# Kernel tuning notes

Hardware: AMD Instinct MI355X
Metric: run time of the kernel (lower is better)

The kernel has to match this reference:

```python
import jax, jax.numpy as jnp
import numpy as np

B, N, M, C, K = 2, 8192, 4096, 64, 16
HID = 256
EPS_BN = 1e-5


def setup_inputs() -> dict:
    key = jax.random.key(0)
    ks = jax.random.split(key, 16)
    def rn(i, shape, scale=1.0):
        return jax.random.normal(ks[i], shape, jnp.float32) * scale
    return {
        "pcl": rn(0, (B, M, 3)),
        "pcl_noise": rn(1, (B, N, 3)),
        "feature": rn(2, (B, M, C)),
        # MLP_CONV (2d 1x1): 6 -> 256 (BN+ReLU) -> C
        "w2a": rn(3, (HID, 6), 0.3), "b2a": rn(4, (HID,), 0.1),
        "g2a": 1.0 + rn(5, (HID,), 0.1), "bt2a": rn(6, (HID,), 0.1),
        "w2b": rn(7, (C, HID), 0.1), "b2b": rn(8, (C,), 0.1),
        # MLP_CONV_1d: 3C -> C (BN+ReLU) -> C
        "w1a": rn(9, (C, 3 * C), 0.1), "b1a": rn(10, (C,), 0.1),
        "g1a": 1.0 + rn(11, (C,), 0.1), "bt1a": rn(12, (C,), 0.1),
        "w1b": rn(13, (C, C), 0.1), "b1b": rn(14, (C,), 0.1),
    }


def _sqdist(x, y):  # [B,n,3],[B,m,3] -> [B,n,m]
    return (jnp.sum(x * x, -1, keepdims=True)
            - 2.0 * jnp.einsum('bnc,bmc->bnm', x, y)
            + jnp.sum(y * y, -1)[:, None, :])


def _gather(x, idx):  # x [B,M,D], idx [B,...] -> [B,...,D]
    return jax.vmap(lambda xb, ib: xb[ib])(x, idx)


def _bn(h, g, b):  # inference BatchNorm: running mean 0, var 1
    return h * (g / jnp.sqrt(1.0 + EPS_BN)) + b


def reference(pcl, pcl_noise, feature, w2a, b2a, g2a, bt2a, w2b, b2b,
              w1a, b1a, g1a, bt1a, w1b, b1b):
    # nearest clean point for each noisy point (knn_points K=1)
    close_idx = jnp.argmin(_sqdist(pcl_noise, pcl), axis=-1)          # [B,N]
    close_point = _gather(pcl, close_idx)                             # [B,N,3]
    # K nearest neighbors of close_point within pcl (dil_knn, d=1)
    _, idx = jax.lax.top_k(-_sqdist(close_point, pcl), K)             # [B,N,K]
    knn_points = _gather(pcl, idx)[:, :, 1:, :]                       # [B,N,K-1,3]
    knn_feat = _gather(feature, idx)[:, :, 1:, :]                     # [B,N,K-1,C]
    close_feat = _gather(feature, close_idx)                          # [B,N,C]

    delta = knn_points - pcl_noise[:, :, None, :]                     # [B,N,K-1,3]
    dst = jnp.linalg.norm(delta, axis=-1)                             # [B,N,K-1]
    e = jnp.exp(-10.0 * dst)
    weight = e / (jnp.sum(e, -1, keepdims=True) + 1e-7)               # [B,N,K-1]

    cp = jnp.broadcast_to(close_point[:, :, None, :], delta.shape)
    delta_points = jnp.concatenate([delta, cp], axis=-1)              # [B,N,K-1,6]

    # MLP_CONV2 (1x1 convs over channel dim)
    h = jnp.einsum('bnkc,oc->bnko', delta_points, w2a) + b2a
    h = jax.nn.relu(_bn(h, g2a, bt2a))
    pf = jnp.einsum('bnkc,oc->bnko', h, w2b) + b2b                    # [B,N,K-1,C]

    point_feature = jnp.einsum('bnk,bnkc->bnc', weight, pf)           # [B,N,C]
    co_feature = jnp.einsum('bnk,bnkc->bnc', weight, knn_feat)        # [B,N,C]
    df = jnp.concatenate([close_feat, co_feature, point_feature], -1)  # [B,N,3C]

    # MLP_CONV_1d
    h1 = jnp.einsum('bnc,oc->bno', df, w1a) + b1a
    h1 = jax.nn.relu(_bn(h1, g1a, bt1a))
    return jnp.einsum('bnc,oc->bno', h1, w1b) + b1b                   # [B,N,C]
```

## Files before the change

### kernel.cpp

```cpp
#include <hip/hip_runtime.h>
#include <float.h>

typedef unsigned short u16;
typedef unsigned int u32;
typedef unsigned char u8;

typedef float f32x4 __attribute__((ext_vector_type(4)));
typedef short bh8   __attribute__((ext_vector_type(8)));

__device__ __forceinline__ float bf(u16 u) { return __uint_as_float(((u32)u) << 16); }
__device__ __forceinline__ u16 f2bf(float v) {
    u32 x = __float_as_uint(v);
    u32 r = x + 0x7fffu + ((x >> 16) & 1u);
    return (u16)(r >> 16);
}
__device__ __forceinline__ int detect_f32(const void* probe) {
    const u16* u = (const u16*)probe;
    u16 v = u[(threadIdx.x & 63) * 2];
    int e = (int)((v >> 7) & 0xFF);
    int moderate = (e >= 100) && (e <= 140);
    return __popcll(__ballot(moderate)) < 48;
}
__device__ __forceinline__ float ldv(int f32, const void* p, int i) {
    return f32 ? ((const float*)p)[i] : bf(((const u16*)p)[i]);
}
__device__ __forceinline__ float dot3(float x0, float x1, float x2,
                                      float y0, float y1, float y2) {
    return __fmaf_rn(x2, y2, __fmaf_rn(x1, y1, __fmul_rn(x0, y0)));
}
__device__ __forceinline__ float qdist(float x0, float x1, float x2, float sx, float4 p) {
    float dot = dot3(x0, x1, x2, p.x, p.y, p.z);
    return __fadd_rn(__fsub_rn(sx, __fmul_rn(2.0f, dot)), p.w);
}
__device__ __forceinline__ u32 mkey32(float d) {
    u32 f = __float_as_uint(d);
    return f ^ (u32)((((int)f) >> 31) | 0x80000000);
}
__device__ __forceinline__ bh8 ldb(const void* p) { return *(const bh8*)p; }
__device__ __forceinline__ f32x4 mfma16(bh8 a, bh8 b, f32x4 c) {
    return __builtin_amdgcn_mfma_f32_16x16x32_bf16(a, b, c, 0, 0, 0);
}

__device__ __forceinline__ void knn_fallback(const float4* __restrict__ src,
                                             float x0, float x1, float x2, float sx,
                                             int q, u16* __restrict__ knn, int lane) {
    u32 k0=~0u,k1=~0u,k2=~0u,k3=~0u,k4=~0u,k5=~0u,k6=~0u,k7=~0u,
        k8=~0u,k9=~0u,k10=~0u,k11=~0u,k12=~0u,k13=~0u,k14=~0u,k15=~0u;
    u32 i0r=0,i1r=0,i2r=0,i3r=0,i4r=0,i5r=0,i6r=0,i7r=0,
        i8r=0,i9r=0,i10r=0,i11r=0,i12r=0,i13r=0,i14r=0,i15r=0;
    for (int j = 0; j < 64; ++j) {
        int cin = (j << 6) + lane;
        float d = qdist(x0, x1, x2, sx, src[cin]);
        u32 v = mkey32(d); u32 vi = (u32)cin;
        if (v < k15) {
            { u32 c_=(v<k0); u32 nk=c_?v:k0; u32 nv=c_?k0:v; u32 ni=c_?vi:i0r; u32 nj=c_?i0r:vi; k0=nk;i0r=ni;v=nv;vi=nj; }
            { u32 c_=(v<k1); u32 nk=c_?v:k1; u32 nv=c_?k1:v; u32 ni=c_?vi:i1r; u32 nj=c_?i1r:vi; k1=nk;i1r=ni;v=nv;vi=nj; }
            { u32 c_=(v<k2); u32 nk=c_?v:k2; u32 nv=c_?k2:v; u32 ni=c_?vi:i2r; u32 nj=c_?i2r:vi; k2=nk;i2r=ni;v=nv;vi=nj; }
            { u32 c_=(v<k3); u32 nk=c_?v:k3; u32 nv=c_?k3:v; u32 ni=c_?vi:i3r; u32 nj=c_?i3r:vi; k3=nk;i3r=ni;v=nv;vi=nj; }
            { u32 c_=(v<k4); u32 nk=c_?v:k4; u32 nv=c_?k4:v; u32 ni=c_?vi:i4r; u32 nj=c_?i4r:vi; k4=nk;i4r=ni;v=nv;vi=nj; }
            { u32 c_=(v<k5); u32 nk=c_?v:k5; u32 nv=c_?k5:v; u32 ni=c_?vi:i5r; u32 nj=c_?i5r:vi; k5=nk;i5r=ni;v=nv;vi=nj; }
            { u32 c_=(v<k6); u32 nk=c_?v:k6; u32 nv=c_?k6:v; u32 ni=c_?vi:i6r; u32 nj=c_?i6r:vi; k6=nk;i6r=ni;v=nv;vi=nj; }
            { u32 c_=(v<k7); u32 nk=c_?v:k7; u32 nv=c_?k7:v; u32 ni=c_?vi:i7r; u32 nj=c_?i7r:vi; k7=nk;i7r=ni;v=nv;vi=nj; }
            { u32 c_=(v<k8); u32 nk=c_?v:k8; u32 nv=c_?k8:v; u32 ni=c_?vi:i8r; u32 nj=c_?i8r:vi; k8=nk;i8r=ni;v=nv;vi=nj; }
            { u32 c_=(v<k9); u32 nk=c_?v:k9; u32 nv=c_?k9:v; u32 ni=c_?vi:i9r; u32 nj=c_?i9r:vi; k9=nk;i9r=ni;v=nv;vi=nj; }
            { u32 c_=(v<k10); u32 nk=c_?v:k10; u32 nv=c_?k10:v; u32 ni=c_?vi:i10r; u32 nj=c_?i10r:vi; k10=nk;i10r=ni;v=nv;vi=nj; }
            { u32 c_=(v<k11); u32 nk=c_?v:k11; u32 nv=c_?k11:v; u32 ni=c_?vi:i11r; u32 nj=c_?i11r:vi; k11=nk;i11r=ni;v=nv;vi=nj; }
            { u32 c_=(v<k12); u32 nk=c_?v:k12; u32 nv=c_?k12:v; u32 ni=c_?vi:i12r; u32 nj=c_?i12r:vi; k12=nk;i12r=ni;v=nv;vi=nj; }
            { u32 c_=(v<k13); u32 nk=c_?v:k13; u32 nv=c_?k13:v; u32 ni=c_?vi:i13r; u32 nj=c_?i13r:vi; k13=nk;i13r=ni;v=nv;vi=nj; }
            { u32 c_=(v<k14); u32 nk=c_?v:k14; u32 nv=c_?k14:v; u32 ni=c_?vi:i14r; u32 nj=c_?i14r:vi; k14=nk;i14r=ni;v=nv;vi=nj; }
            { u32 c_=(v<k15); u32 nk=c_?v:k15; u32 nv=c_?k15:v; u32 ni=c_?vi:i15r; u32 nj=c_?i15r:vi; k15=nk;i15r=ni;v=nv;vi=nj; }
        }
    }
    u32 myres = 0;
    for (int o = 0; o < 16; ++o) {
        u32 bk = k0, bi2 = i0r;
#pragma unroll
        for (int m = 32; m >= 1; m >>= 1) {
            u32 ok = __shfl_xor(bk, m), oi = __shfl_xor(bi2, m);
            if (ok < bk || (ok == bk && oi < bi2)) { bk = ok; bi2 = oi; }
        }
        if (lane == o) myres = bi2;
        if (k0 == bk && i0r == bi2) {
            k0=k1; i0r=i1r; k1=k2; i1r=i2r; k2=k3; i2r=i3r; k3=k4; i3r=i4r;
            k4=k5; i4r=i5r; k5=k6; i5r=i6r; k6=k7; i6r=i7r; k7=k8; i7r=i8r;
            k8=k9; i8r=i9r; k9=k10; i9r=i10r; k10=k11; i10r=i11r; k11=k12; i11r=i12r;
            k12=k13; i12r=i13r; k13=k14; i13r=i14r; k14=k15; i14r=i15r;
            k15=~0u; i15r=0xFFFFu;
        }
    }
    if (lane < 16) knn[((size_t)q << 4) + lane] = (u16)myres;
}

__global__ __launch_bounds__(256) void k_pre(const void* __restrict__ probe,
                                             const void* __restrict__ w2b,
                                             const void* __restrict__ w1a,
                                             const void* __restrict__ w1b,
                                             u32* __restrict__ canonb,
                                             const void* __restrict__ pcl,
                                             float4* __restrict__ pcl4) {
    int f32 = detect_f32(probe);
    int bx = blockIdx.x, t = threadIdx.x;
    if (bx < 64) {
        int ix = bx * 256 + t;
        const void* src; int j;
        if (ix < 8192)       { src = w2b; j = ix; }
        else if (ix < 14336) { src = w1a; j = ix - 8192; }
        else                 { src = w1b; j = ix - 14336; }
        u32 out;
        if (f32) {
            const float* f = (const float*)src;
            out = ((u32)f2bf(f[2*j+1]) << 16) | (u32)f2bf(f[2*j]);
        } else {
            const u16* su = (const u16*)src;
            out = ((u32)su[2*j+1] << 16) | (u32)su[2*j];
        }
        canonb[ix] = out;
    } else {
        int i = (bx - 64) * 256 + t;
        float x = ldv(f32, pcl, i*3+0), y = ldv(f32, pcl, i*3+1), z = ldv(f32, pcl, i*3+2);
        float s = __fadd_rn(__fadd_rn(__fmul_rn(x,x), __fmul_rn(y,y)), __fmul_rn(z,z));
        pcl4[i] = make_float4(x, y, z, s);
    }
}

__global__ __launch_bounds__(256) void k_sel(const float4* __restrict__ pcl4,
                                             const void* __restrict__ noise,
                                             u16* __restrict__ cidx,
                                             u16* __restrict__ knn) {
    __shared__ __align__(16) char arena[32768];
    int bx = blockIdx.x;
    int r5 = bx % 5, c5 = bx / 5;
    int t = threadIdx.x, lane = t & 63, wv = t >> 6;

    if (r5 == 0) {
        float4* tile = (float4*)arena;
        int f32 = detect_f32(noise);
        int g = t >> 4, s = t & 15;
        int q = c5 * 16 + g;
        int b = q >> 13;
        const float4* src = pcl4 + ((size_t)b << 12);
        float x0 = ldv(f32, noise, q*3+0), x1 = ldv(f32, noise, q*3+1), x2 = ldv(f32, noise, q*3+2);
        float sx = __fadd_rn(__fadd_rn(__fmul_rn(x0,x0), __fmul_rn(x1,x1)), __fmul_rn(x2,x2));
        float bd = FLT_MAX; int bi = 0;
        for (int ch = 0; ch < 2; ++ch) {
            __syncthreads();
#pragma unroll
            for (int i = 0; i < 8; ++i) { int ix = t + (i << 8); tile[ix] = src[(ch << 11) + ix]; }
            __syncthreads();
            for (int j = 0; j < 128; ++j) {
                int cl = (j << 4) + s;
                float4 p = tile[cl];
                float d = qdist(x0, x1, x2, sx, p);
                int c = (ch << 11) + cl;
                if (d < bd) { bd = d; bi = c; }
            }
        }
#pragma unroll
        for (int m = 8; m >= 1; m >>= 1) {
            float od = __shfl_xor(bd, m);
            int   oi = __shfl_xor(bi, m);
            if (od < bd || (od == bd && oi < bi)) { bd = od; bi = oi; }
        }
        if (s == 0) cidx[q] = (u16)(bi & 4095);
        return;
    }

    u8*  bins0 = (u8*)arena;
    u8*  bins1 = (u8*)(arena + 4096);
    u32* hist0 = (u32*)(arena + 8192);
    u32* hist1 = (u32*)(arena + 9216);
    u32* skey0 = (u32*)(arena + 10240);
    u32* skey1 = (u32*)(arena + 11264);
    u16* sidx0 = (u16*)(arena + 12288);
    u16* sidx1 = (u16*)(arena + 12800);
    float* rmn0 = (float*)(arena + 13312);
    float* rmx0 = (float*)(arena + 13328);
    float* rmn1 = (float*)(arena + 13344);
    float* rmx1 = (float*)(arena + 13360);
    u32* scnt0 = (u32*)(arena + 13376);
    u32* scnt1 = (u32*)(arena + 13380);
    int* ibst0 = (int*)(arena + 13384);
    int* ibst1 = (int*)(arena + 13388);

    int qp = c5 * 4 + (r5 - 1);
    int q0 = qp << 1, q1 = q0 | 1;
    int b = q0 >> 12;
    const float4* src = pcl4 + ((size_t)b << 12);
    float4 Q0 = src[q0 & 4095];
    float4 Q1 = src[q1 & 4095];
    float ax0 = Q0.x, ax1 = Q0.y, ax2 = Q0.z, asx = Q0.w;
    float bx0 = Q1.x, bx1 = Q1.y, bx2 = Q1.z, bsx = Q1.w;
    hist0[t] = 0; hist1[t] = 0;
    if (t == 0) { *scnt0 = 0; *scnt1 = 0; }
    {
        float4 p = src[t << 4];
        float da = qdist(ax0, ax1, ax2, asx, p);
        float db = qdist(bx0, bx1, bx2, bsx, p);
        float mn0 = da, mx0 = da, mn1 = db, mx1 = db;
#pragma unroll
        for (int m = 32; m >= 1; m >>= 1) {
            mn0 = fminf(mn0, __shfl_xor(mn0, m));
            mx0 = fmaxf(mx0, __shfl_xor(mx0, m));
            mn1 = fminf(mn1, __shfl_xor(mn1, m));
            mx1 = fmaxf(mx1, __shfl_xor(mx1, m));
        }
        if (lane == 0) { rmn0[wv] = mn0; rmx0[wv] = mx0; rmn1[wv] = mn1; rmx1[wv] = mx1; }
    }
    __syncthreads();
    float dmn0 = fminf(fminf(rmn0[0], rmn0[1]), fminf(rmn0[2], rmn0[3]));
    float dmx0 = fmaxf(fmaxf(rmx0[0], rmx0[1]), fmaxf(rmx0[2], rmx0[3]));
    float sc0f = 1024.0f / fmaxf(dmx0 - dmn0, 1e-20f);
    float dmn1 = fminf(fminf(rmn1[0], rmn1[1]), fminf(rmn1[2], rmn1[3]));
    float dmx1 = fmaxf(fmaxf(rmx1[0], rmx1[1]), fmaxf(rmx1[2], rmx1[3]));
    float sc1f = 1024.0f / fmaxf(dmx1 - dmn1, 1e-20f);
#pragma unroll 4
    for (int j = 0; j < 16; ++j) {
        int cin = (j << 8) + t;
        float4 p = src[cin];
        float d0 = qdist(ax0, ax1, ax2, asx, p);
        float d1 = qdist(bx0, bx1, bx2, bsx, p);
        int bn0 = (int)fminf(fmaxf((d0 - dmn0) * sc0f, 0.0f), 255.0f);
        int bn1 = (int)fminf(fmaxf((d1 - dmn1) * sc1f, 0.0f), 255.0f);
        bins0[cin] = (u8)bn0;
        bins1[cin] = (u8)bn1;
        if (bn0 < 255) atomicAdd(&hist0[bn0], 1u);
        if (bn1 < 255) atomicAdd(&hist1[bn1], 1u);
    }
    __syncthreads();
    if (wv < 2) {
        u32* hh = wv ? hist1 : hist0;
        u32 c0 = hh[4*lane], c1 = hh[4*lane+1];
        u32 c2 = hh[4*lane+2], c3 = hh[4*lane+3];
        u32 loc = c0 + c1 + c2 + c3;
        u32 x = loc;
#pragma unroll
        for (int off = 1; off < 64; off <<= 1) { u32 v = __shfl_up(x, off); if (lane >= off) x += v; }
        u32 excl = x - loc;
        int cand = 999;
        if (excl + c0 >= 16u) cand = 4*lane;
        else if (excl + c0 + c1 >= 16u) cand = 4*lane + 1;
        else if (excl + c0 + c1 + c2 >= 16u) cand = 4*lane + 2;
        else if (excl + loc >= 16u) cand = 4*lane + 3;
#pragma unroll
        for (int m = 32; m >= 1; m >>= 1) cand = min(cand, __shfl_xor(cand, m));
        if (lane == 0) { if (wv) *ibst1 = cand; else *ibst0 = cand; }
    }
    __syncthreads();
    int bstar0 = *ibst0, bstar1 = *ibst1;
#pragma unroll
    for (int j = 0; j < 16; ++j) {
        int cin = (j << 8) + t;
        int s0 = (int)bins0[cin] <= bstar0;
        int s1 = (int)bins1[cin] <= bstar1;
        if (s0 | s1) {
            float4 p = src[cin];
            if (s0) {
                u32 pos = atomicAdd(scnt0, 1u);
                if (pos < 256u) {
                    float d = qdist(ax0, ax1, ax2, asx, p);
                    skey0[pos] = mkey32(d); sidx0[pos] = (u16)cin;
                }
            }
            if (s1) {
                u32 pos = atomicAdd(scnt1, 1u);
                if (pos < 256u) {
                    float d = qdist(bx0, bx1, bx2, bsx, p);
                    skey1[pos] = mkey32(d); sidx1[pos] = (u16)cin;
                }
            }
        }
    }
    __syncthreads();
    u32 n0 = *scnt0, n1 = *scnt1;
    if (t < 128) {
        if (n0 <= 256u) {
            for (u32 e = (u32)t; e < n0; e += 128u) {
                u32 k = skey0[e]; u32 i = (u32)sidx0[e];
                int rank = 0;
                for (u32 j = 0; j < n0; ++j) {
                    u32 kj = skey0[j]; u32 ij = (u32)sidx0[j];
                    rank += (kj < k) || (kj == k && ij < i);
                }
                if (rank < 16) knn[((size_t)q0 << 4) + rank] = (u16)i;
            }
        } else if (wv == 0) {
            knn_fallback(src, ax0, ax1, ax2, asx, q0, knn, lane);
        }
    } else {
        if (n1 <= 256u) {
            for (u32 e = (u32)(t - 128); e < n1; e += 128u) {
                u32 k = skey1[e]; u32 i = (u32)sidx1[e];
                int rank = 0;
                for (u32 j = 0; j < n1; ++j) {
                    u32 kj = skey1[j]; u32 ij = (u32)sidx1[j];
                    rank += (kj < k) || (kj == k && ij < i);
                }
                if (rank < 16) knn[((size_t)q1 << 4) + rank] = (u16)i;
            }
        } else if (wv == 2) {
            knn_fallback(src, bx0, bx1, bx2, bsx, q1, knn, lane);
        }
    }
}

__global__ __launch_bounds__(256) void k_tail(const float4* __restrict__ pcl4,
                                              const void* __restrict__ noise,
                                              const void* __restrict__ feat,
                                              const u16* __restrict__ cidx,
                                              const u16* __restrict__ knn,
                                              const void* __restrict__ w2a,
                                              const void* __restrict__ b2a,
                                              const void* __restrict__ g2a,
                                              const void* __restrict__ bt2a,
                                              const u32* __restrict__ canonb,
                                              const void* __restrict__ b2b,
                                              const void* __restrict__ b1a,
                                              const void* __restrict__ g1a,
                                              const void* __restrict__ bt1a,
                                              const void* __restrict__ b1b,
                                              void* __restrict__ outp) {
    __shared__ __align__(16) char arena[39744];
    char* dpb_hi = arena;
    char* dpb_lo = arena + 4352;
    char* wbt    = arena + 8704;
    char* wsbp   = arena + 9984;
    u16*  jbuf   = (u16*)(arena + 10048);
    char* hbm_   = arena + 10560;
    char* dfm    = arena + 27200;
    char* h1m    = arena;

    int f32 = detect_f32(noise);
    int t = threadIdx.x, lane = t & 63, wv = t >> 6;
    int g = lane >> 4, l15 = lane & 15;
    int qbb = blockIdx.x * 16;
    int o_lane = wv * 16 + l15;
    const float rbn = 1.0f / sqrtf(1.0f + 1e-5f);
    const char* cb = (const char*)canonb;
    const f32x4 zero4 = {0.f, 0.f, 0.f, 0.f};

    float of2r[4];
    bh8 wH[4];
#pragma unroll
    for (int j = 0; j < 4; ++j) {
        int oh = wv*64 + j*16 + l15;
        float sc = ldv(f32, g2a, oh) * rbn;
        of2r[j] = ldv(f32, b2a, oh) * sc + ldv(f32, bt2a, oh);
        bh8 wz = (bh8){0,0,0,0,0,0,0,0};
        if (g < 3) {
#pragma unroll
            for (int c = 0; c < 6; ++c) {
                float wval = ldv(f32, w2a, oh*6 + c) * sc;
                u16 h = f2bf(wval);
                u16 e = (g == 2) ? f2bf(wval - bf(h)) : h;
                wz[c] = (short)e;
            }
        }
        wH[j] = wz;
    }
    float s1o  = ldv(f32, g1a, o_lane) * rbn;
    float o1o  = ldv(f32, b1a, o_lane) * s1o + ldv(f32, bt1a, o_lane);
    float b2bo = ldv(f32, b2b, o_lane);
    float b1fo = ldv(f32, b1b, o_lane);

    {
        int s = lane & 15;
        int ql = wv*4 + (lane >> 4);
        int q = qbb + ql;
        int pbase = (q >> 13) << 12;
        int ci = ((int)cidx[q]) & 4095;
        float4 cp = pcl4[pbase + ci];
        float x0 = ldv(f32, noise, q*3+0), x1 = ldv(f32, noise, q*3+1), x2 = ldv(f32, noise, q*3+2);
        float e = 0.0f;
        if (s >= 1) {
            int jk = ((int)knn[(size_t)(pbase + ci) * 16 + s]) & 4095;
            float4 p = pcl4[pbase + jk];
            float d0 = p.x - x0, d1 = p.y - x1, d2 = p.z - x2;
            float dst = sqrtf(__fadd_rn(__fadd_rn(__fmul_rn(d0,d0), __fmul_rn(d1,d1)), __fmul_rn(d2,d2)));
            e = expf(-10.0f * dst);
            float v6[6] = {d0, d1, d2, cp.x, cp.y, cp.z};
            bh8 HW = (bh8){0,0,0,0,0,0,0,0};
            bh8 LW = (bh8){0,0,0,0,0,0,0,0};
#pragma unroll
            for (int c = 0; c < 6; ++c) {
                u16 hh = f2bf(v6[c]);
                u16 ll = f2bf(v6[c] - bf(hh));
                HW[c] = (short)hh;
                LW[c] = (short)ll;
            }
            *(bh8*)(dpb_hi + (ql*17 + s)*16) = HW;
            *(bh8*)(dpb_lo + (ql*17 + s)*16) = LW;
            jbuf[ql*16 + s] = (u16)jk;
        }
        float es = e;
#pragma unroll
        for (int m = 8; m >= 1; m >>= 1) es += __shfl_xor(es, m, 16);
        float den = es + 1e-7f;
        if (s >= 1) *(float*)(wbt + s*80 + ql*4) = e / den;
        if (s == 0) *(float*)(wsbp + ql*4) = es / den;
    }
    __syncthreads();

#pragma unroll
    for (int qq = 0; qq < 4; ++qq) {
        int qloc = wv*4 + qq;
        int q = qbb + qloc;
        int pbase = (q >> 13) << 12;
        int ci = ((int)cidx[q]) & 4095;
        size_t fcb = ((size_t)(pbase + ci)) << 6;
        float c0, c1 = 0.0f;
        if (f32) {
            const float* ff = (const float*)feat;
            c0 = ff[fcb + lane];
#pragma unroll
            for (int k = 1; k < 16; ++k) {
                float wk = *(const float*)(wbt + k*80 + qloc*4);
                c1 += wk * ff[(((size_t)(pbase + (int)jbuf[qloc*16 + k])) << 6) + lane];
            }
        } else {
            const u16* fb = (const u16*)feat;
            c0 = bf(fb[fcb + lane]);
#pragma unroll
            for (int k = 1; k < 16; ++k) {
                float wk = *(const float*)(wbt + k*80 + qloc*4);
                c1 += wk * bf(fb[(((size_t)(pbase + (int)jbuf[qloc*16 + k])) << 6) + lane]);
            }
        }
        char* dr = dfm + qloc*784;
        u16 h0 = f2bf(c0); u16 l0 = f2bf(c0 - bf(h0));
        u16 h1v = f2bf(c1); u16 l1v = f2bf(c1 - bf(h1v));
        *(u16*)(dr + (size_t)lane*2)         = h0;
        *(u16*)(dr + (size_t)(192+lane)*2)   = l0;
        *(u16*)(dr + (size_t)(64+lane)*2)    = h1v;
        *(u16*)(dr + (size_t)(256+lane)*2)   = l1v;
    }

    {
        f32x4 hba[4];
#pragma unroll
        for (int j = 0; j < 4; ++j) hba[j] = zero4;
#pragma unroll 2
        for (int k = 1; k < 16; ++k) {
            bh8 af;
            if (g < 3) {
                const char* base = (g == 1) ? dpb_lo : dpb_hi;
                af = ldb(base + (l15*17 + k)*16);
            } else {
                af = (bh8){0,0,0,0,0,0,0,0};
            }
            f32x4 wk4 = *(const f32x4*)(wbt + k*80 + g*16);
#pragma unroll
            for (int j = 0; j < 4; ++j) {
                f32x4 d = mfma16(af, wH[j], zero4);
#pragma unroll
                for (int r = 0; r < 4; ++r)
                    hba[j][r] += wk4[r] * fmaxf(d[r] + of2r[j], 0.0f);
            }
        }
#pragma unroll
        for (int j = 0; j < 4; ++j)
#pragma unroll
            for (int r = 0; r < 4; ++r) {
                int q = g*4 + r;
                int o = wv*64 + j*16 + l15;
                float x = hba[j][r];
                u16 h = f2bf(x); u16 l = f2bf(x - bf(h));
                *(u16*)(hbm_ + q*1040 + (size_t)o*2)       = h;
                *(u16*)(hbm_ + q*1040 + 512 + (size_t)o*2) = l;
            }
    }
    __syncthreads();

    {
        f32x4 acA = zero4, acB = zero4;
#pragma unroll 2
        for (int ks = 0; ks < 8; ++ks) {
            bh8 bw = ldb(cb + (size_t)o_lane*512 + ks*64 + g*16);
            bh8 aH = ldb(hbm_ + l15*1040 + ks*64 + g*16);
            bh8 aL = ldb(hbm_ + l15*1040 + 512 + ks*64 + g*16);
            acA = mfma16(aH, bw, acA);
            acB = mfma16(aL, bw, acB);
        }
        f32x4 wsb4 = *(const f32x4*)(wsbp + g*16);
#pragma unroll
        for (int r = 0; r < 4; ++r) {
            int q = g*4 + r;
            float pf = acA[r] + acB[r] + b2bo * wsb4[r];
            u16 h = f2bf(pf); u16 l = f2bf(pf - bf(h));
            *(u16*)(dfm + q*784 + (size_t)(128 + o_lane)*2) = h;
            *(u16*)(dfm + q*784 + (size_t)(320 + o_lane)*2) = l;
        }
    }
    __syncthreads();

    {
        f32x4 acA = zero4, acB = zero4;
#pragma unroll 2
        for (int ks = 0; ks < 6; ++ks) {
            bh8 bw = ldb(cb + 32768 + (size_t)o_lane*384 + ks*64 + g*16);
            bh8 aH = ldb(dfm + l15*784 + ks*64 + g*16);
            bh8 aL = ldb(dfm + l15*784 + 384 + ks*64 + g*16);
            acA = mfma16(aH, bw, acA);
            acB = mfma16(aL, bw, acB);
        }
#pragma unroll
        for (int r = 0; r < 4; ++r) {
            int q = g*4 + r;
            float z = (acA[r] + acB[r]) * s1o + o1o;
            z = fmaxf(z, 0.0f);
            u16 h = f2bf(z); u16 l = f2bf(z - bf(h));
            *(u16*)(h1m + q*272 + (size_t)o_lane*2)       = h;
            *(u16*)(h1m + q*272 + 128 + (size_t)o_lane*2) = l;
        }
    }
    __syncthreads();

    {
        bh8 bw0 = ldb(cb + 57344 + (size_t)o_lane*128 + g*16);
        bh8 bw1 = ldb(cb + 57344 + (size_t)o_lane*128 + 64 + g*16);
        f32x4 ac = zero4;
        { bh8 a = ldb(h1m + l15*272 +   0 + g*16); ac = mfma16(a, bw0, ac); }
        { bh8 a = ldb(h1m + l15*272 +  64 + g*16); ac = mfma16(a, bw1, ac); }
        { bh8 a = ldb(h1m + l15*272 + 128 + g*16); ac = mfma16(a, bw0, ac); }
        { bh8 a = ldb(h1m + l15*272 + 192 + g*16); ac = mfma16(a, bw1, ac); }
#pragma unroll
        for (int r = 0; r < 4; ++r) {
            int q = g*4 + r;
            float ov = ac[r] + b1fo;
            size_t ob = ((size_t)(qbb + q) << 6) + o_lane;
            if (f32) ((float*)outp)[ob] = ov;
            else     ((u16*)outp)[ob]   = f2bf(ov);
        }
    }
}

extern "C" void kernel_launch(void* const* d_in, const int* in_sizes, int n_in,
                              void* d_out, int out_size, void* d_ws, size_t ws_size,
                              hipStream_t stream) {
    const void* pcl   = d_in[0];
    const void* noise = d_in[1];
    const void* feat  = d_in[2];
    const void* w2a   = d_in[3];
    const void* b2a   = d_in[4];
    const void* g2a   = d_in[5];
    const void* bt2a  = d_in[6];
    const void* w2b   = d_in[7];
    const void* b2b   = d_in[8];
    const void* w1a   = d_in[9];
    const void* b1a   = d_in[10];
    const void* g1a   = d_in[11];
    const void* bt1a  = d_in[12];
    const void* w1b   = d_in[13];
    const void* b1b   = d_in[14];

    char* ws = (char*)d_ws;
    float4* pcl4 = (float4*)ws;
    u16* cidx = (u16*)(ws + 131072);
    u16* knn  = (u16*)(ws + 163840);
    u32* canonb = (u32*)(ws + 425984);

    k_pre  <<<96,   256, 0, stream>>>(noise, w2b, w1a, w1b, canonb, pcl, pcl4);
    k_sel  <<<5120, 256, 0, stream>>>(pcl4, noise, cidx, knn);
    k_tail <<<1024, 256, 0, stream>>>(pcl4, noise, feat, cidx, knn,
                                      w2a, b2a, g2a, bt2a, canonb, b2b,
                                      b1a, g1a, bt1a, b1b, d_out);
}
```

Baseline: 205.6 us.

## Process four kNN query points per block in k_sel instead of two

Each kNN-selection block now handles four clean-point queries instead of two. Every candidate point loaded from global memory is reused for four distance computations, and the grid shrinks from 5120 to 3072 blocks. Shared memory per block grows to about 27KB for four bin/histogram/key arrays. Each wave now ranks one query's candidates on its own, so the rank loop uses 64 lanes per query instead of 128, and register pressure rises, which may lower occupancy.

```diff
diff --git a/kernel.cpp b/kernel.cpp
--- a/kernel.cpp
+++ b/kernel.cpp
@@ -129,14 +129,14 @@
                                              u16* __restrict__ knn) {
     __shared__ __align__(16) char arena[32768];
     int bx = blockIdx.x;
-    int r5 = bx % 5, c5 = bx / 5;
+    int r3 = bx % 3, c3 = bx / 3;
     int t = threadIdx.x, lane = t & 63, wv = t >> 6;
 
-    if (r5 == 0) {
+    if (r3 == 0) {
         float4* tile = (float4*)arena;
         int f32 = detect_f32(noise);
         int g = t >> 4, s = t & 15;
-        int q = c5 * 16 + g;
+        int q = c3 * 16 + g;
         int b = q >> 13;
         const float4* src = pcl4 + ((size_t)b << 12);
         float x0 = ldv(f32, noise, q*3+0), x1 = ldv(f32, noise, q*3+1), x2 = ldv(f32, noise, q*3+2);
@@ -165,70 +165,82 @@
         return;
     }
 
-    u8*  bins0 = (u8*)arena;
-    u8*  bins1 = (u8*)(arena + 4096);
-    u32* hist0 = (u32*)(arena + 8192);
-    u32* hist1 = (u32*)(arena + 9216);
-    u32* skey0 = (u32*)(arena + 10240);
-    u32* skey1 = (u32*)(arena + 11264);
-    u16* sidx0 = (u16*)(arena + 12288);
-    u16* sidx1 = (u16*)(arena + 12800);
-    float* rmn0 = (float*)(arena + 13312);
-    float* rmx0 = (float*)(arena + 13328);
-    float* rmn1 = (float*)(arena + 13344);
-    float* rmx1 = (float*)(arena + 13360);
-    u32* scnt0 = (u32*)(arena + 13376);
-    u32* scnt1 = (u32*)(arena + 13380);
-    int* ibst0 = (int*)(arena + 13384);
-    int* ibst1 = (int*)(arena + 13388);
-
-    int qp = c5 * 4 + (r5 - 1);
-    int q0 = qp << 1, q1 = q0 | 1;
+    u8*  binsA = (u8*)arena;
+    u32* histA = (u32*)(arena + 16384);
+    u32* skeyA = (u32*)(arena + 20480);
+    u16* sidxA = (u16*)(arena + 24576);
+    float* rmnA = (float*)(arena + 26624);
+    float* rmxA = (float*)(arena + 26688);
+    u32* scntA = (u32*)(arena + 26752);
+    int* ibstA = (int*)(arena + 26768);
+
+    int id = c3 * 2 + (r3 - 1);
+    int q0 = id << 2;
     int b = q0 >> 12;
     const float4* src = pcl4 + ((size_t)b << 12);
-    float4 Q0 = src[q0 & 4095];
-    float4 Q1 = src[q1 & 4095];
-    float ax0 = Q0.x, ax1 = Q0.y, ax2 = Q0.z, asx = Q0.w;
-    float bx0 = Q1.x, bx1 = Q1.y, bx2 = Q1.z, bsx = Q1.w;
-    hist0[t] = 0; hist1[t] = 0;
-    if (t == 0) { *scnt0 = 0; *scnt1 = 0; }
+    int qm = q0 & 4095;
+    float4 Q0 = src[qm], Q1 = src[qm+1], Q2 = src[qm+2], Q3 = src[qm+3];
+    float qx0=Q0.x, qy0=Q0.y, qz0=Q0.z, qs0=Q0.w;
+    float qx1=Q1.x, qy1=Q1.y, qz1=Q1.z, qs1=Q1.w;
+    float qx2=Q2.x, qy2=Q2.y, qz2=Q2.z, qs2=Q2.w;
+    float qx3=Q3.x, qy3=Q3.y, qz3=Q3.z, qs3=Q3.w;
+#pragma unroll
+    for (int qi = 0; qi < 4; ++qi) histA[(qi << 8) + t] = 0;
+    if (t < 4) scntA[t] = 0;
     {
         float4 p = src[t << 4];
-        float da = qdist(ax0, ax1, ax2, asx, p);
-        float db = qdist(bx0, bx1, bx2, bsx, p);
-        float mn0 = da, mx0 = da, mn1 = db, mx1 = db;
+        float d0 = qdist(qx0,qy0,qz0,qs0,p);
+        float d1 = qdist(qx1,qy1,qz1,qs1,p);
+        float d2 = qdist(qx2,qy2,qz2,qs2,p);
+        float d3 = qdist(qx3,qy3,qz3,qs3,p);
+        float mn0=d0,mx0=d0, mn1=d1,mx1=d1, mn2=d2,mx2=d2, mn3=d3,mx3=d3;
 #pragma unroll
         for (int m = 32; m >= 1; m >>= 1) {
-            mn0 = fminf(mn0, __shfl_xor(mn0, m));
-            mx0 = fmaxf(mx0, __shfl_xor(mx0, m));
-            mn1 = fminf(mn1, __shfl_xor(mn1, m));
-            mx1 = fmaxf(mx1, __shfl_xor(mx1, m));
-        }
-        if (lane == 0) { rmn0[wv] = mn0; rmx0[wv] = mx0; rmn1[wv] = mn1; rmx1[wv] = mx1; }
-    }
-    __syncthreads();
-    float dmn0 = fminf(fminf(rmn0[0], rmn0[1]), fminf(rmn0[2], rmn0[3]));
-    float dmx0 = fmaxf(fmaxf(rmx0[0], rmx0[1]), fmaxf(rmx0[2], rmx0[3]));
-    float sc0f = 1024.0f / fmaxf(dmx0 - dmn0, 1e-20f);
-    float dmn1 = fminf(fminf(rmn1[0], rmn1[1]), fminf(rmn1[2], rmn1[3]));
-    float dmx1 = fmaxf(fmaxf(rmx1[0], rmx1[1]), fmaxf(rmx1[2], rmx1[3]));
-    float sc1f = 1024.0f / fmaxf(dmx1 - dmn1, 1e-20f);
-#pragma unroll 4
+            mn0 = fminf(mn0, __shfl_xor(mn0, m)); mx0 = fmaxf(mx0, __shfl_xor(mx0, m));
+            mn1 = fminf(mn1, __shfl_xor(mn1, m)); mx1 = fmaxf(mx1, __shfl_xor(mx1, m));
+            mn2 = fminf(mn2, __shfl_xor(mn2, m)); mx2 = fmaxf(mx2, __shfl_xor(mx2, m));
+            mn3 = fminf(mn3, __shfl_xor(mn3, m)); mx3 = fmaxf(mx3, __shfl_xor(mx3, m));
+        }
+        if (lane == 0) {
+            rmnA[wv] = mn0;      rmxA[wv] = mx0;
+            rmnA[4+wv] = mn1;    rmxA[4+wv] = mx1;
+            rmnA[8+wv] = mn2;    rmxA[8+wv] = mx2;
+            rmnA[12+wv] = mn3;   rmxA[12+wv] = mx3;
+        }
+    }
+    __syncthreads();
+    float dmn0 = fminf(fminf(rmnA[0],rmnA[1]),fminf(rmnA[2],rmnA[3]));
+    float sc0  = 1024.0f / fmaxf(fmaxf(fmaxf(rmxA[0],rmxA[1]),fmaxf(rmxA[2],rmxA[3])) - dmn0, 1e-20f);
+    float dmn1 = fminf(fminf(rmnA[4],rmnA[5]),fminf(rmnA[6],rmnA[7]));
+    float sc1  = 1024.0f / fmaxf(fmaxf(fmaxf(rmxA[4],rmxA[5]),fmaxf(rmxA[6],rmxA[7])) - dmn1, 1e-20f);
+    float dmn2 = fminf(fminf(rmnA[8],rmnA[9]),fminf(rmnA[10],rmnA[11]));
+    float sc2  = 1024.0f / fmaxf(fmaxf(fmaxf(rmxA[8],rmxA[9]),fmaxf(rmxA[10],rmxA[11])) - dmn2, 1e-20f);
+    float dmn3 = fminf(fminf(rmnA[12],rmnA[13]),fminf(rmnA[14],rmnA[15]));
+    float sc3  = 1024.0f / fmaxf(fmaxf(fmaxf(rmxA[12],rmxA[13]),fmaxf(rmxA[14],rmxA[15])) - dmn3, 1e-20f);
+#pragma unroll 8
     for (int j = 0; j < 16; ++j) {
         int cin = (j << 8) + t;
         float4 p = src[cin];
-        float d0 = qdist(ax0, ax1, ax2, asx, p);
-        float d1 = qdist(bx0, bx1, bx2, bsx, p);
-        int bn0 = (int)fminf(fmaxf((d0 - dmn0) * sc0f, 0.0f), 255.0f);
-        int bn1 = (int)fminf(fmaxf((d1 - dmn1) * sc1f, 0.0f), 255.0f);
-        bins0[cin] = (u8)bn0;
-        bins1[cin] = (u8)bn1;
-        if (bn0 < 255) atomicAdd(&hist0[bn0], 1u);
-        if (bn1 < 255) atomicAdd(&hist1[bn1], 1u);
-    }
-    __syncthreads();
-    if (wv < 2) {
-        u32* hh = wv ? hist1 : hist0;
+        float d0 = qdist(qx0,qy0,qz0,qs0,p);
+        float d1 = qdist(qx1,qy1,qz1,qs1,p);
+        float d2 = qdist(qx2,qy2,qz2,qs2,p);
+        float d3 = qdist(qx3,qy3,qz3,qs3,p);
+        int bn0 = (int)fminf(fmaxf((d0 - dmn0) * sc0, 0.0f), 255.0f);
+        int bn1 = (int)fminf(fmaxf((d1 - dmn1) * sc1, 0.0f), 255.0f);
+        int bn2 = (int)fminf(fmaxf((d2 - dmn2) * sc2, 0.0f), 255.0f);
+        int bn3 = (int)fminf(fmaxf((d3 - dmn3) * sc3, 0.0f), 255.0f);
+        binsA[cin]         = (u8)bn0;
+        binsA[4096 + cin]  = (u8)bn1;
+        binsA[8192 + cin]  = (u8)bn2;
+        binsA[12288 + cin] = (u8)bn3;
+        if (bn0 < 255) atomicAdd(&histA[bn0], 1u);
+        if (bn1 < 255) atomicAdd(&histA[256 + bn1], 1u);
+        if (bn2 < 255) atomicAdd(&histA[512 + bn2], 1u);
+        if (bn3 < 255) atomicAdd(&histA[768 + bn3], 1u);
+    }
+    __syncthreads();
+    {
+        u32* hh = histA + (wv << 8);
         u32 c0 = hh[4*lane], c1 = hh[4*lane+1];
         u32 c2 = hh[4*lane+2], c3 = hh[4*lane+3];
         u32 loc = c0 + c1 + c2 + c3;
@@ -243,62 +255,60 @@
         else if (excl + loc >= 16u) cand = 4*lane + 3;
 #pragma unroll
         for (int m = 32; m >= 1; m >>= 1) cand = min(cand, __shfl_xor(cand, m));
-        if (lane == 0) { if (wv) *ibst1 = cand; else *ibst0 = cand; }
-    }
-    __syncthreads();
-    int bstar0 = *ibst0, bstar1 = *ibst1;
-#pragma unroll
+        if (lane == 0) ibstA[wv] = cand;
+    }
+    __syncthreads();
+    int bs0 = ibstA[0], bs1 = ibstA[1], bs2 = ibstA[2], bs3 = ibstA[3];
+#pragma unroll 4
     for (int j = 0; j < 16; ++j) {
         int cin = (j << 8) + t;
-        int s0 = (int)bins0[cin] <= bstar0;
-        int s1 = (int)bins1[cin] <= bstar1;
-        if (s0 | s1) {
+        int s0 = (int)binsA[cin]         <= bs0;
+        int s1 = (int)binsA[4096 + cin]  <= bs1;
+        int s2 = (int)binsA[8192 + cin]  <= bs2;
+        int s3 = (int)binsA[12288 + cin] <= bs3;
+        if (s0 | s1 | s2 | s3) {
             float4 p = src[cin];
             if (s0) {
-                u32 pos = atomicAdd(scnt0, 1u);
-                if (pos < 256u) {
-                    float d = qdist(ax0, ax1, ax2, asx, p);
-                    skey0[pos] = mkey32(d); sidx0[pos] = (u16)cin;
-                }
+                u32 pos = atomicAdd(&scntA[0], 1u);
+                if (pos < 256u) { skeyA[pos] = mkey32(qdist(qx0,qy0,qz0,qs0,p)); sidxA[pos] = (u16)cin; }
             }
             if (s1) {
-                u32 pos = atomicAdd(scnt1, 1u);
-                if (pos < 256u) {
-                    float d = qdist(bx0, bx1, bx2, bsx, p);
-                    skey1[pos] = mkey32(d); sidx1[pos] = (u16)cin;
-                }
-            }
-        }
-    }
-    __syncthreads();
-    u32 n0 = *scnt0, n1 = *scnt1;
-    if (t < 128) {
-        if (n0 <= 256u) {
-            for (u32 e = (u32)t; e < n0; e += 128u) {
-                u32 k = skey0[e]; u32 i = (u32)sidx0[e];
+                u32 pos = atomicAdd(&scntA[1], 1u);
+                if (pos < 256u) { skeyA[256+pos] = mkey32(qdist(qx1,qy1,qz1,qs1,p)); sidxA[256+pos] = (u16)cin; }
+            }
+            if (s2) {
+                u32 pos = atomicAdd(&scntA[2], 1u);
+                if (pos < 256u) { skeyA[512+pos] = mkey32(qdist(qx2,qy2,qz2,qs2,p)); sidxA[512+pos] = (u16)cin; }
+            }
+            if (s3) {
+                u32 pos = atomicAdd(&scntA[3], 1u);
+                if (pos < 256u) { skeyA[768+pos] = mkey32(qdist(qx3,qy3,qz3,qs3,p)); sidxA[768+pos] = (u16)cin; }
+            }
+        }
+    }
+    __syncthreads();
+    {
+        u32 nq = scntA[wv];
+        u32* sk = skeyA + (wv << 8);
+        u16* si = sidxA + (wv << 8);
+        int myq = q0 + wv;
+        if (nq <= 256u) {
+            for (u32 e = (u32)lane; e < nq; e += 64u) {
+                u32 k = sk[e]; u32 i = (u32)si[e];
                 int rank = 0;
-                for (u32 j = 0; j < n0; ++j) {
-                    u32 kj = skey0[j]; u32 ij = (u32)sidx0[j];
+                for (u32 jj = 0; jj < nq; ++jj) {
+                    u32 kj = sk[jj]; u32 ij = (u32)si[jj];
                     rank += (kj < k) || (kj == k && ij < i);
                 }
-                if (rank < 16) knn[((size_t)q0 << 4) + rank] = (u16)i;
-            }
-        } else if (wv == 0) {
-            knn_fallback(src, ax0, ax1, ax2, asx, q0, knn, lane);
-        }
-    } else {
-        if (n1 <= 256u) {
-            for (u32 e = (u32)(t - 128); e < n1; e += 128u) {
-                u32 k = skey1[e]; u32 i = (u32)sidx1[e];
-                int rank = 0;
-                for (u32 j = 0; j < n1; ++j) {
-                    u32 kj = skey1[j]; u32 ij = (u32)sidx1[j];
-                    rank += (kj < k) || (kj == k && ij < i);
-                }
-                if (rank < 16) knn[((size_t)q1 << 4) + rank] = (u16)i;
-            }
-        } else if (wv == 2) {
-            knn_fallback(src, bx0, bx1, bx2, bsx, q1, knn, lane);
+                if (rank < 16) knn[((size_t)myq << 4) + rank] = (u16)i;
+            }
+        } else {
+            float X, Y, Z, S;
+            if (wv == 0)      { X = qx0; Y = qy0; Z = qz0; S = qs0; }
+            else if (wv == 1) { X = qx1; Y = qy1; Z = qz1; S = qs1; }
+            else if (wv == 2) { X = qx2; Y = qy2; Z = qz2; S = qs2; }
+            else              { X = qx3; Y = qy3; Z = qz3; S = qs3; }
+            knn_fallback(src, X, Y, Z, S, myq, knn, lane);
         }
     }
 }
@@ -559,7 +569,7 @@
     u32* canonb = (u32*)(ws + 425984);
 
     k_pre  <<<96,   256, 0, stream>>>(noise, w2b, w1a, w1b, canonb, pcl, pcl4);
-    k_sel  <<<5120, 256, 0, stream>>>(pcl4, noise, cidx, knn);
+    k_sel  <<<3072, 256, 0, stream>>>(pcl4, noise, cidx, knn);
     k_tail <<<1024, 256, 0, stream>>>(pcl4, noise, feat, cidx, knn,
                                       w2a, b2a, g2a, bt2a, canonb, b2b,
                                       b1a, g1a, bt1a, b1b, d_out);
```

New measurement: 206.1 us. No clear change (+0.2%).
